# Performance work log

Hardware: AMD Instinct MI355X
Metric: run time of the kernel (lower is better)

The kernel has to match this reference:

```python
import jax, jax.numpy as jnp
import numpy as np

N, D_IN, D_OUT, H = 8192, 256, 128, 2
SLOPE = 0.2
EPS = 1e-5  # InstanceNorm2d default eps


def setup_inputs() -> dict:
    key = jax.random.key(0)
    ks = jax.random.split(key, 6)
    x = jax.random.normal(ks[0], (N, D_IN), dtype=jnp.float32)
    conn_mask = jnp.where(jax.random.uniform(ks[1], (N, N)) < 0.05, 0.0, -1e9).astype(jnp.float32)
    W = jax.random.normal(ks[2], (H, D_IN, D_OUT), dtype=jnp.float32) * 0.05
    a_src = jax.random.normal(ks[3], (H, D_OUT), dtype=jnp.float32) * 0.1
    a_tgt = jax.random.normal(ks[4], (H, D_OUT), dtype=jnp.float32) * 0.1
    W_res = jax.random.normal(ks[5], (D_OUT, D_IN), dtype=jnp.float32) * 0.05
    return {"x": x, "conn_mask": conn_mask, "W": W, "a_src": a_src, "a_tgt": a_tgt, "W_res": W_res}


def reference(x, conn_mask, W, a_src, a_tgt, W_res):
    # dropout is identity in eval mode
    proj = jnp.einsum('nd,hdf->hnf', x, W)                      # [H,N,F]
    s_src = jnp.einsum('hnf,hf->hn', proj, a_src)[:, :, None]   # [H,N,1]
    s_tgt = jnp.einsum('hnf,hf->hn', proj, a_tgt)[:, None, :]   # [H,1,N]
    scores = jax.nn.leaky_relu(s_src + s_tgt, negative_slope=SLOPE)  # [H,N,N]
    attn = jax.nn.softmax(conn_mask[None] + scores, axis=1)     # softmax over dim=1 as in torch code
    vals = jnp.einsum('hmn,hnf->hmf', attn, proj)               # bmm -> [H,N,F]
    vals = vals.mean(axis=0)                                    # head mean -> [N,F]
    # InstanceNorm2d(1, affine=False) over the whole [N,F] plane, biased variance
    mu = vals.mean()
    var = jnp.mean(jnp.square(vals - mu))
    vals_norm = (vals - mu) / jnp.sqrt(var + EPS)
    out = vals_norm + x @ W_res.T                               # residual projection (no bias)
    out = jax.nn.elu(out)
    return (out, conn_mask)
```

## Files before the change

kernel.cpp:

```cpp
#include <hip/hip_runtime.h>
#include <stdint.h>

#define NN   8192
#define DIN  256
#define FF   128
#define NF   (NN*FF)
#define SLOPE 0.2f
#define EPSI  1e-5f

typedef float vf4 __attribute__((ext_vector_type(4)));

#define OFF_PROJ   0
#define OFF_RESID  (2*NF)
#define OFF_PACKED (3*NF)
#define OFF_SS     (4*NF)
#define OFF_ST     (OFF_SS + 2*NN)
#define OFF_CSUM   (OFF_ST + 2*NN)
#define OFF_STATS  (OFF_CSUM + 2*NN)
#define OFF_NTAB   (OFF_STATS + 16)
#define OFF_VALS   (OFF_NTAB + 4*NN)
#define OFF_WT     (OFF_VALS + NF)

__device__ __forceinline__ float lrelu(float x) { return x >= 0.f ? x : SLOPE * x; }

__device__ __forceinline__ uint32_t bfpack(float a, float b) {
  uint32_t ua = __float_as_uint(a); ua += 0x7fffu + ((ua >> 16) & 1u);
  uint32_t ub = __float_as_uint(b); ub += 0x7fffu + ((ub >> 16) & 1u);
  return (ua >> 16) | (ub & 0xffff0000u);
}

__global__ __launch_bounds__(256) void k_wt(const float* __restrict__ wres, float* __restrict__ wt) {
  int i = blockIdx.x * 256 + threadIdx.x;
  int d = i >> 7, f = i & 127;
  wt[i] = wres[f * DIN + d];
}

__global__ __launch_bounds__(256) void k_gemm(const float* __restrict__ x, const float* __restrict__ Wh,
                                              const float* __restrict__ wt, float* __restrict__ proj,
                                              float* __restrict__ resid) {
  const int h = blockIdx.y;
  const float* __restrict__ Wsrc = (h < 2) ? (Wh + h * (DIN * FF)) : wt;
  float* __restrict__ outp = (h < 2) ? (proj + h * NF) : resid;
  const int row0 = blockIdx.x * 64;
  __shared__ float xs[64 * 68];
  const int tid = threadIdx.x;
  const int ft = tid & 15, rt = tid >> 4;
  const int f0 = ft * 8, r0 = rt * 4;
  float acc[4][8];
#pragma unroll
  for (int j = 0; j < 4; ++j)
#pragma unroll
    for (int k = 0; k < 8; ++k) acc[j][k] = 0.f;

  for (int kc = 0; kc < 4; ++kc) {
    const int d0 = kc * 64;
#pragma unroll
    for (int k2 = 0; k2 < 4; ++k2) {
      int i = tid * 4 + k2 * 1024;
      int r = i >> 6, dd = i & 63;
      *(float4*)&xs[r * 68 + dd] = *(const float4*)&x[(row0 + r) * DIN + d0 + dd];
    }
    __syncthreads();
#pragma unroll
    for (int g = 0; g < 16; ++g) {
      const int dd = g * 4;
      float xr[4][4];
#pragma unroll
      for (int j = 0; j < 4; ++j) {
        float4 t = *(const float4*)&xs[(r0 + j) * 68 + dd];
        xr[j][0] = t.x; xr[j][1] = t.y; xr[j][2] = t.z; xr[j][3] = t.w;
      }
#pragma unroll
      for (int i = 0; i < 4; ++i) {
        float4 wa = *(const float4*)&Wsrc[(d0 + dd + i) * FF + f0];
        float4 wb = *(const float4*)&Wsrc[(d0 + dd + i) * FF + f0 + 4];
#pragma unroll
        for (int j = 0; j < 4; ++j) {
          float xx = xr[j][i];
          acc[j][0] += xx * wa.x; acc[j][1] += xx * wa.y; acc[j][2] += xx * wa.z; acc[j][3] += xx * wa.w;
          acc[j][4] += xx * wb.x; acc[j][5] += xx * wb.y; acc[j][6] += xx * wb.z; acc[j][7] += xx * wb.w;
        }
      }
    }
    __syncthreads();
  }
#pragma unroll
  for (int j = 0; j < 4; ++j) {
    int row = row0 + r0 + j;
    *(float4*)&outp[row * FF + f0]     = make_float4(acc[j][0], acc[j][1], acc[j][2], acc[j][3]);
    *(float4*)&outp[row * FF + f0 + 4] = make_float4(acc[j][4], acc[j][5], acc[j][6], acc[j][7]);
  }
}

__global__ __launch_bounds__(256) void k_sprep(const float* __restrict__ proj, const float* __restrict__ a_src,
                                               const float* __restrict__ a_tgt, float* __restrict__ ss,
                                               float* __restrict__ st, uint32_t* __restrict__ packed) {
  int lane = threadIdx.x & 63, wid = threadIdx.x >> 6;
  int n = blockIdx.x * 4 + wid;
  float2 q0 = *(const float2*)&proj[n * FF + 2 * lane];
  float2 q1 = *(const float2*)&proj[NF + n * FF + 2 * lane];
  float2 as0 = *(const float2*)&a_src[2 * lane];
  float2 at0 = *(const float2*)&a_tgt[2 * lane];
  float2 as1 = *(const float2*)&a_src[FF + 2 * lane];
  float2 at1 = *(const float2*)&a_tgt[FF + 2 * lane];
  float v0 = q0.x * as0.x + q0.y * as0.y;
  float v1 = q0.x * at0.x + q0.y * at0.y;
  float v2 = q1.x * as1.x + q1.y * as1.y;
  float v3 = q1.x * at1.x + q1.y * at1.y;
#pragma unroll
  for (int o = 1; o < 64; o <<= 1) {
    v0 += __shfl_xor(v0, o); v1 += __shfl_xor(v1, o);
    v2 += __shfl_xor(v2, o); v3 += __shfl_xor(v3, o);
  }
  uint2 pk;
  pk.x = bfpack(q0.x, q1.x);
  pk.y = bfpack(q0.y, q1.y);
  *(uint2*)&packed[n * FF + 2 * lane] = pk;
  if (lane == 0) { ss[n] = v0; ss[NN + n] = v2; st[n] = v1; st[NN + n] = v3; }
}

__global__ __launch_bounds__(256) void k_scan(const float* __restrict__ mask, float* __restrict__ maskout,
                                              const float* __restrict__ ss, const float* __restrict__ st,
                                              float* __restrict__ csum, uint32_t* __restrict__ bitmask) {
  const int tid = threadIdx.x;
  const int lane = tid & 63, wv = tid >> 6;
  const int n = blockIdx.x * 256 + tid;
  const int m0 = blockIdx.y * 128;
  const int wbase = blockIdx.x * 8 + wv * 2;
  const float st0 = st[n], st1 = st[NN + n];
  float c0 = 0.f, c1 = 0.f;

  for (int i = 0; i < 128; i += 4) {
    float v[4];
#pragma unroll
    for (int r = 0; r < 4; ++r)
      v[r] = __builtin_nontemporal_load(&mask[(size_t)(m0 + i + r) * NN + n]);
#pragma unroll
    for (int r = 0; r < 4; ++r) {
      const int m = m0 + i + r;
      __builtin_nontemporal_store(v[r], &maskout[(size_t)m * NN + n]);
      bool e = v[r] > -0.5e9f;
      unsigned long long bm = __ballot(e);
      if (lane == 0)
        *(uint2*)&bitmask[m * 256 + wbase] = make_uint2((uint32_t)bm, (uint32_t)(bm >> 32));
      float w0 = __expf(lrelu(ss[m] + st0));
      float w1 = __expf(lrelu(ss[NN + m] + st1));
      c0 += e ? w0 : 0.f;
      c1 += e ? w1 : 0.f;
    }
  }
  atomicAdd(&csum[n], c0);
  atomicAdd(&csum[NN + n], c1);
}

__global__ __launch_bounds__(256) void k_ntab(const float* __restrict__ st, const float* __restrict__ csum,
                                              float4* __restrict__ ntab) {
  int i = blockIdx.x * 256 + threadIdx.x;
  ntab[i] = make_float4(st[i], st[NN + i], 1.f / csum[i], 1.f / csum[NN + i]);
}

__global__ __launch_bounds__(256) void k_vals(const uint32_t* __restrict__ bitmask, const uint32_t* __restrict__ packed,
                                              const float4* __restrict__ ntab, const float* __restrict__ ss,
                                              float* __restrict__ vals, float* __restrict__ stats) {
  __shared__ uint16_t el[4][1024];
  const int lane = threadIdx.x & 63, wid = threadIdx.x >> 6;
  const int m = blockIdx.x * 4 + wid;

  uint4 wv = ((const uint4*)(bitmask + m * 256))[lane];
  uint32_t wd[4] = {wv.x, wv.y, wv.z, wv.w};
  int cnt = __popc(wd[0]) + __popc(wd[1]) + __popc(wd[2]) + __popc(wd[3]);
  int pre = cnt;
#pragma unroll
  for (int o = 1; o < 64; o <<= 1) { int t = __shfl_up(pre, o); if (lane >= o) pre += t; }
  int nE = __shfl(pre, 63);
  int base = pre - cnt;
#pragma unroll
  for (int u = 0; u < 4; ++u) {
    uint32_t w = wd[u];
    int nbase = lane * 128 + u * 32;
    while (w) {
      int b = __builtin_ctz(w); w &= w - 1;
      if (base < 1024) el[wid][base] = (uint16_t)(nbase + b);
      ++base;
    }
  }
  if (nE > 1024) nE = 1024;
  __builtin_amdgcn_wave_barrier();

  const float ss0 = ss[m], ss1 = ss[NN + m];
  float a00 = 0.f, a01 = 0.f, a10 = 0.f, a11 = 0.f;
  const char* __restrict__ pb = (const char*)packed;
  const int lane8 = 8 * lane;
  for (int t = 0; t < nE; t += 64) {
    int e = t + lane;
    float w0 = 0.f, w1 = 0.f; uint32_t off = 0;
    if (e < nE) {
      int n = el[wid][e];
      float4 tb = ntab[n];
      w0 = __expf(lrelu(ss0 + tb.x)) * tb.z;
      w1 = __expf(lrelu(ss1 + tb.y)) * tb.w;
      off = (uint32_t)n << 9;
    }
#pragma unroll 1
    for (int k2 = 0; k2 < 4; ++k2) {
      uint2 d[16];
#pragma unroll
      for (int j = 0; j < 16; ++j) {
        uint32_t so = __builtin_amdgcn_readlane(off, k2 * 16 + j);
        d[j] = *(const uint2*)(pb + so + lane8);
      }
#pragma unroll
      for (int j = 0; j < 16; ++j) {
        float sw0 = __uint_as_float(__builtin_amdgcn_readlane(__float_as_uint(w0), k2 * 16 + j));
        float sw1 = __uint_as_float(__builtin_amdgcn_readlane(__float_as_uint(w1), k2 * 16 + j));
        uint32_t pa = d[j].x, pc = d[j].y;
        a00 += sw0 * __uint_as_float(pa << 16);
        a10 += sw1 * __uint_as_float(pa & 0xffff0000u);
        a01 += sw0 * __uint_as_float(pc << 16);
        a11 += sw1 * __uint_as_float(pc & 0xffff0000u);
      }
    }
  }

  float v0 = 0.5f * (a00 + a10), v1 = 0.5f * (a01 + a11);
  *(float2*)&vals[m * FF + 2 * lane] = make_float2(v0, v1);
  float s = v0 + v1, q = v0 * v0 + v1 * v1;
#pragma unroll
  for (int o = 1; o < 64; o <<= 1) { s += __shfl_xor(s, o); q += __shfl_xor(q, o); }
  if (lane == 0) { atomicAdd(stats, s); atomicAdd(stats + 1, q); }
}

__global__ __launch_bounds__(256) void k_final(const float* __restrict__ vals, const float* __restrict__ resid,
                                               const float* __restrict__ stats, float* __restrict__ out) {
  int i = (blockIdx.x * 256 + threadIdx.x) * 4;
  float mu = stats[0] * (1.f / NF);
  float var = stats[1] * (1.f / NF) - mu * mu;
  float rs = rsqrtf(var + EPSI);
  float4 v = *(const float4*)&vals[i];
  float4 r = *(const float4*)&resid[i];
  float t0 = (v.x - mu) * rs + r.x;
  float t1 = (v.y - mu) * rs + r.y;
  float t2 = (v.z - mu) * rs + r.z;
  float t3 = (v.w - mu) * rs + r.w;
  float4 o;
  o.x = t0 > 0.f ? t0 : expm1f(t0);
  o.y = t1 > 0.f ? t1 : expm1f(t1);
  o.z = t2 > 0.f ? t2 : expm1f(t2);
  o.w = t3 > 0.f ? t3 : expm1f(t3);
  *(float4*)&out[i] = o;
}

extern "C" void kernel_launch(void* const* d_in, const int* in_sizes, int n_in,
                              void* d_out, int out_size, void* d_ws, size_t ws_size,
                              hipStream_t stream) {
  const float* x     = (const float*)d_in[0];
  const float* mask  = (const float*)d_in[1];
  const float* W     = (const float*)d_in[2];
  const float* a_src = (const float*)d_in[3];
  const float* a_tgt = (const float*)d_in[4];
  const float* wres  = (const float*)d_in[5];
  float* out = (float*)d_out;
  float* wsf = (float*)d_ws;

  float*    proj    = wsf + OFF_PROJ;
  uint32_t* bitmask = (uint32_t*)(wsf + OFF_PROJ);
  float*    resid   = wsf + OFF_RESID;
  uint32_t* packed  = (uint32_t*)(wsf + OFF_PACKED);
  float*    ss      = wsf + OFF_SS;
  float*    st      = wsf + OFF_ST;
  float*    csum    = wsf + OFF_CSUM;
  float*    stats   = wsf + OFF_STATS;
  float4*   ntab    = (float4*)(wsf + OFF_NTAB);
  float*    vals    = wsf + OFF_VALS;
  float*    wt      = wsf + OFF_WT;

  (void)hipMemsetAsync(csum, 0, (2 * NN + 16) * sizeof(float), stream);

  hipLaunchKernelGGL(k_wt,    dim3(DIN * FF / 256), dim3(256), 0, stream, wres, wt);
  hipLaunchKernelGGL(k_gemm,  dim3(NN / 64, 3),     dim3(256), 0, stream, x, W, wt, proj, resid);
  hipLaunchKernelGGL(k_sprep, dim3(NN / 4),         dim3(256), 0, stream, proj, a_src, a_tgt, ss, st, packed);
  hipLaunchKernelGGL(k_scan,  dim3(NN / 256, NN / 128), dim3(256), 0, stream, mask, out + NF, ss, st, csum, bitmask);
  hipLaunchKernelGGL(k_ntab,  dim3(NN / 256),       dim3(256), 0, stream, st, csum, ntab);
  hipLaunchKernelGGL(k_vals,  dim3(NN / 4),         dim3(256), 0, stream, bitmask, packed, ntab, ss, vals, stats);
  hipLaunchKernelGGL(k_final, dim3(NF / 1024),      dim3(256), 0, stream, vals, resid, stats, out);
}
```

Measured before the change: 769.2 us.

## Double-buffer gathered rows into LDS via async global_load_lds in k_vals

In k_vals, the gather of packed bf16 projection rows now goes through direct global-to-LDS loads into a per-wave double buffer, with explicit waitcnt fences so the next sub-block's loads overlap the FMAs on the current one. Per-edge weights are staged in LDS rather than broadcast with readlane. In k_scan, the ss values are loaded once per lane and broadcast with readlane instead of being reloaded every row, and the unroll grows from 4 to 8. This adds LDS pressure, which may cut occupancy, and relies on hand-tuned waitcnt encodings that are easy to get wrong.

```diff
diff --git a/kernel.cpp b/kernel.cpp
--- a/kernel.cpp
+++ b/kernel.cpp
@@ -9,6 +9,15 @@
 #define EPSI  1e-5f
 
 typedef float vf4 __attribute__((ext_vector_type(4)));
+
+#if __has_builtin(__builtin_amdgcn_sched_barrier)
+#define SCHED_FENCE() __builtin_amdgcn_sched_barrier(0)
+#else
+#define SCHED_FENCE() asm volatile("" ::: "memory")
+#endif
+
+#define WAITCNT_VM16_LGKM0 0x4070
+#define WAITCNT_VM0_LGKM0  0x0070
 
 #define OFF_PROJ   0
 #define OFF_RESID  (2*NF)
@@ -128,23 +137,30 @@
   const int m0 = blockIdx.y * 128;
   const int wbase = blockIdx.x * 8 + wv * 2;
   const float st0 = st[n], st1 = st[NN + n];
+  const float ssA = ss[m0 + lane],      ssB = ss[m0 + 64 + lane];
+  const float ssC = ss[NN + m0 + lane], ssD = ss[NN + m0 + 64 + lane];
   float c0 = 0.f, c1 = 0.f;
 
-  for (int i = 0; i < 128; i += 4) {
-    float v[4];
-#pragma unroll
-    for (int r = 0; r < 4; ++r)
+  for (int i = 0; i < 128; i += 8) {
+    float v[8];
+#pragma unroll
+    for (int r = 0; r < 8; ++r)
       v[r] = __builtin_nontemporal_load(&mask[(size_t)(m0 + i + r) * NN + n]);
 #pragma unroll
-    for (int r = 0; r < 4; ++r) {
+    for (int r = 0; r < 8; ++r) {
       const int m = m0 + i + r;
       __builtin_nontemporal_store(v[r], &maskout[(size_t)m * NN + n]);
       bool e = v[r] > -0.5e9f;
       unsigned long long bm = __ballot(e);
       if (lane == 0)
         *(uint2*)&bitmask[m * 256 + wbase] = make_uint2((uint32_t)bm, (uint32_t)(bm >> 32));
-      float w0 = __expf(lrelu(ss[m] + st0));
-      float w1 = __expf(lrelu(ss[NN + m] + st1));
+      const int ri = i + r;
+      float s0 = __uint_as_float(__builtin_amdgcn_readlane(
+                   __float_as_uint(ri < 64 ? ssA : ssB), ri & 63));
+      float s1 = __uint_as_float(__builtin_amdgcn_readlane(
+                   __float_as_uint(ri < 64 ? ssC : ssD), ri & 63));
+      float w0 = __expf(lrelu(s0 + st0));
+      float w1 = __expf(lrelu(s1 + st1));
       c0 += e ? w0 : 0.f;
       c1 += e ? w1 : 0.f;
     }
@@ -163,6 +179,8 @@
                                               const float4* __restrict__ ntab, const float* __restrict__ ss,
                                               float* __restrict__ vals, float* __restrict__ stats) {
   __shared__ uint16_t el[4][1024];
+  __shared__ uint32_t dbuf[4][2][8 * 128];
+  __shared__ float2   wbuf[4][64];
   const int lane = threadIdx.x & 63, wid = threadIdx.x >> 6;
   const int m = blockIdx.x * 4 + wid;
 
@@ -190,7 +208,9 @@
   const float ss0 = ss[m], ss1 = ss[NN + m];
   float a00 = 0.f, a01 = 0.f, a10 = 0.f, a11 = 0.f;
   const char* __restrict__ pb = (const char*)packed;
-  const int lane8 = 8 * lane;
+  uint32_t* __restrict__ db0 = &dbuf[wid][0][0];
+  uint32_t* __restrict__ db1 = &dbuf[wid][1][0];
+
   for (int t = 0; t < nE; t += 64) {
     int e = t + lane;
     float w0 = 0.f, w1 = 0.f; uint32_t off = 0;
@@ -201,25 +221,55 @@
       w1 = __expf(lrelu(ss1 + tb.y)) * tb.w;
       off = (uint32_t)n << 9;
     }
+    wbuf[wid][lane] = make_float2(w0, w1);
+    __builtin_amdgcn_wave_barrier();
+
+#define ISSUE_SB(sb)                                                                   \
+    {                                                                                  \
+      uint32_t* dst = ((sb) & 1) ? db1 : db0;                                          \
+      _Pragma("unroll")                                                                \
+      for (int j = 0; j < 8; ++j) {                                                    \
+        uint32_t so = __builtin_amdgcn_readlane(off, (sb) * 8 + j);                    \
+        const uint32_t* g = (const uint32_t*)(pb + so) + lane;                         \
+        __builtin_amdgcn_global_load_lds(                                              \
+            (const __attribute__((address_space(1))) uint32_t*)g,                      \
+            (__attribute__((address_space(3))) uint32_t*)&dst[j * 128], 4, 0, 0);      \
+        __builtin_amdgcn_global_load_lds(                                              \
+            (const __attribute__((address_space(1))) uint32_t*)(g + 64),               \
+            (__attribute__((address_space(3))) uint32_t*)&dst[j * 128 + 64], 4, 0, 0); \
+      }                                                                                \
+    }
+
+    ISSUE_SB(0)
 #pragma unroll 1
-    for (int k2 = 0; k2 < 4; ++k2) {
-      uint2 d[16];
-#pragma unroll
-      for (int j = 0; j < 16; ++j) {
-        uint32_t so = __builtin_amdgcn_readlane(off, k2 * 16 + j);
-        d[j] = *(const uint2*)(pb + so + lane8);
+    for (int sb = 0; sb < 8; ++sb) {
+      if (sb < 7) {
+        switch (sb + 1) {
+          case 1: ISSUE_SB(1) break; case 2: ISSUE_SB(2) break; case 3: ISSUE_SB(3) break;
+          case 4: ISSUE_SB(4) break; case 5: ISSUE_SB(5) break; case 6: ISSUE_SB(6) break;
+          case 7: ISSUE_SB(7) break;
+        }
+        SCHED_FENCE();
+        __builtin_amdgcn_s_waitcnt(WAITCNT_VM16_LGKM0);
+        SCHED_FENCE();
+      } else {
+        SCHED_FENCE();
+        __builtin_amdgcn_s_waitcnt(WAITCNT_VM0_LGKM0);
+        SCHED_FENCE();
       }
-#pragma unroll
-      for (int j = 0; j < 16; ++j) {
-        float sw0 = __uint_as_float(__builtin_amdgcn_readlane(__float_as_uint(w0), k2 * 16 + j));
-        float sw1 = __uint_as_float(__builtin_amdgcn_readlane(__float_as_uint(w1), k2 * 16 + j));
-        uint32_t pa = d[j].x, pc = d[j].y;
-        a00 += sw0 * __uint_as_float(pa << 16);
-        a10 += sw1 * __uint_as_float(pa & 0xffff0000u);
-        a01 += sw0 * __uint_as_float(pc << 16);
-        a11 += sw1 * __uint_as_float(pc & 0xffff0000u);
+      const uint32_t* src = (sb & 1) ? db1 : db0;
+#pragma unroll
+      for (int j = 0; j < 8; ++j) {
+        float2 w = wbuf[wid][sb * 8 + j];
+        uint2 d = *(const uint2*)&src[j * 128 + 2 * lane];
+        a00 += w.x * __uint_as_float(d.x << 16);
+        a10 += w.y * __uint_as_float(d.x & 0xffff0000u);
+        a01 += w.x * __uint_as_float(d.y << 16);
+        a11 += w.y * __uint_as_float(d.y & 0xffff0000u);
       }
     }
+    __builtin_amdgcn_wave_barrier();
+#undef ISSUE_SB
   }
 
   float v0 = 0.5f * (a00 + a10), v1 = 0.5f * (a01 + a11);
```

Result: slower. 858.2 us (+11.6%).

## Vectorize mask scan to float4 per thread with interleaved bitmask layout

Applied to the files above, without the earlier changes.

The scan kernel now loads and stores the 256MB connectivity mask as float4 per thread instead of scalar floats, with each block covering 1024 columns by 64 rows. It reads the per-row source scores through readlane broadcasts. Because each ballot now covers every fourth column, the bitmask layout changes, and the vals kernel's index decoding is updated to match. A scheduling barrier is also added between the gather loads and the FMAs in k_vals. The aim is to raise memory-transaction efficiency on the dominant mask copy and scan, at the cost of a more complex bitmask encoding and more atomics per thread.

```diff
diff --git a/kernel.cpp b/kernel.cpp
--- a/kernel.cpp
+++ b/kernel.cpp
@@ -9,6 +9,12 @@
 #define EPSI  1e-5f
 
 typedef float vf4 __attribute__((ext_vector_type(4)));
+
+#if __has_builtin(__builtin_amdgcn_sched_barrier)
+#define SCHED_FENCE() __builtin_amdgcn_sched_barrier(0)
+#else
+#define SCHED_FENCE() asm volatile("" ::: "memory")
+#endif
 
 #define OFF_PROJ   0
 #define OFF_RESID  (2*NF)
@@ -124,33 +130,47 @@
                                               float* __restrict__ csum, uint32_t* __restrict__ bitmask) {
   const int tid = threadIdx.x;
   const int lane = tid & 63, wv = tid >> 6;
-  const int n = blockIdx.x * 256 + tid;
-  const int m0 = blockIdx.y * 128;
-  const int wbase = blockIdx.x * 8 + wv * 2;
-  const float st0 = st[n], st1 = st[NN + n];
-  float c0 = 0.f, c1 = 0.f;
-
-  for (int i = 0; i < 128; i += 4) {
-    float v[4];
-#pragma unroll
-    for (int r = 0; r < 4; ++r)
-      v[r] = __builtin_nontemporal_load(&mask[(size_t)(m0 + i + r) * NN + n]);
-#pragma unroll
-    for (int r = 0; r < 4; ++r) {
+  const int nb = blockIdx.x * 1024 + tid * 4;
+  const int C = blockIdx.x * 4 + wv;
+  const int m0 = blockIdx.y * 64;
+  const vf4 st0 = *(const vf4*)&st[nb];
+  const vf4 st1 = *(const vf4*)&st[NN + nb];
+  const float ssA = ss[m0 + lane];
+  const float ssC = ss[NN + m0 + lane];
+  float c0[4] = {0.f, 0.f, 0.f, 0.f}, c1[4] = {0.f, 0.f, 0.f, 0.f};
+
+  for (int i = 0; i < 64; i += 8) {
+    vf4 v[8];
+#pragma unroll
+    for (int r = 0; r < 8; ++r)
+      v[r] = *(const vf4*)&mask[(size_t)(m0 + i + r) * NN + nb];
+#pragma unroll
+    for (int r = 0; r < 8; ++r) {
       const int m = m0 + i + r;
-      __builtin_nontemporal_store(v[r], &maskout[(size_t)m * NN + n]);
-      bool e = v[r] > -0.5e9f;
-      unsigned long long bm = __ballot(e);
-      if (lane == 0)
-        *(uint2*)&bitmask[m * 256 + wbase] = make_uint2((uint32_t)bm, (uint32_t)(bm >> 32));
-      float w0 = __expf(lrelu(ss[m] + st0));
-      float w1 = __expf(lrelu(ss[NN + m] + st1));
-      c0 += e ? w0 : 0.f;
-      c1 += e ? w1 : 0.f;
-    }
-  }
-  atomicAdd(&csum[n], c0);
-  atomicAdd(&csum[NN + n], c1);
+      __builtin_nontemporal_store(v[r], (vf4*)&maskout[(size_t)m * NN + nb]);
+      unsigned long long bms[4];
+      bool e[4];
+#pragma unroll
+      for (int j = 0; j < 4; ++j) { e[j] = v[r][j] > -0.5e9f; bms[j] = __ballot(e[j]); }
+      if (lane < 8)
+        bitmask[m * 256 + C * 8 + lane] = (uint32_t)(bms[lane >> 1] >> ((lane & 1) * 32));
+      const int ri = i + r;
+      float s0 = __uint_as_float(__builtin_amdgcn_readlane(__float_as_uint(ssA), ri));
+      float s1 = __uint_as_float(__builtin_amdgcn_readlane(__float_as_uint(ssC), ri));
+#pragma unroll
+      for (int j = 0; j < 4; ++j) {
+        float w0 = __expf(lrelu(s0 + st0[j]));
+        float w1 = __expf(lrelu(s1 + st1[j]));
+        c0[j] += e[j] ? w0 : 0.f;
+        c1[j] += e[j] ? w1 : 0.f;
+      }
+    }
+  }
+#pragma unroll
+  for (int j = 0; j < 4; ++j) {
+    atomicAdd(&csum[nb + j], c0[j]);
+    atomicAdd(&csum[NN + nb + j], c1[j]);
+  }
 }
 
 __global__ __launch_bounds__(256) void k_ntab(const float* __restrict__ st, const float* __restrict__ csum,
@@ -177,10 +197,11 @@
 #pragma unroll
   for (int u = 0; u < 4; ++u) {
     uint32_t w = wd[u];
-    int nbase = lane * 128 + u * 32;
+    int widx = 4 * lane + u;
+    int nbase = (widx >> 3) * 256 + (widx & 1) * 128 + ((widx >> 1) & 3);
     while (w) {
       int b = __builtin_ctz(w); w &= w - 1;
-      if (base < 1024) el[wid][base] = (uint16_t)(nbase + b);
+      if (base < 1024) el[wid][base] = (uint16_t)(nbase + 4 * b);
       ++base;
     }
   }
@@ -204,15 +225,17 @@
 #pragma unroll 1
     for (int k2 = 0; k2 < 4; ++k2) {
       uint2 d[16];
+      const int kb = k2 * 16;
 #pragma unroll
       for (int j = 0; j < 16; ++j) {
-        uint32_t so = __builtin_amdgcn_readlane(off, k2 * 16 + j);
+        uint32_t so = __builtin_amdgcn_readlane(off, kb + j);
         d[j] = *(const uint2*)(pb + so + lane8);
       }
+      SCHED_FENCE();
 #pragma unroll
       for (int j = 0; j < 16; ++j) {
-        float sw0 = __uint_as_float(__builtin_amdgcn_readlane(__float_as_uint(w0), k2 * 16 + j));
-        float sw1 = __uint_as_float(__builtin_amdgcn_readlane(__float_as_uint(w1), k2 * 16 + j));
+        float sw0 = __uint_as_float(__builtin_amdgcn_readlane(__float_as_uint(w0), kb + j));
+        float sw1 = __uint_as_float(__builtin_amdgcn_readlane(__float_as_uint(w1), kb + j));
         uint32_t pa = d[j].x, pc = d[j].y;
         a00 += sw0 * __uint_as_float(pa << 16);
         a10 += sw1 * __uint_as_float(pa & 0xffff0000u);
@@ -279,7 +302,7 @@
   hipLaunchKernelGGL(k_wt,    dim3(DIN * FF / 256), dim3(256), 0, stream, wres, wt);
   hipLaunchKernelGGL(k_gemm,  dim3(NN / 64, 3),     dim3(256), 0, stream, x, W, wt, proj, resid);
   hipLaunchKernelGGL(k_sprep, dim3(NN / 4),         dim3(256), 0, stream, proj, a_src, a_tgt, ss, st, packed);
-  hipLaunchKernelGGL(k_scan,  dim3(NN / 256, NN / 128), dim3(256), 0, stream, mask, out + NF, ss, st, csum, bitmask);
+  hipLaunchKernelGGL(k_scan,  dim3(NN / 1024, NN / 64), dim3(256), 0, stream, mask, out + NF, ss, st, csum, bitmask);
   hipLaunchKernelGGL(k_ntab,  dim3(NN / 256),       dim3(256), 0, stream, st, csum, ntab);
   hipLaunchKernelGGL(k_vals,  dim3(NN / 4),         dim3(256), 0, stream, bitmask, packed, ntab, ss, vals, stats);
   hipLaunchKernelGGL(k_final, dim3(NF / 1024),      dim3(256), 0, stream, vals, resid, stats, out);
```

Result: slower. 852.4 us (+10.8%).

## Replace sparse gather aggregation with dense bf16 MFMA over transposed projections

Applied to the files above, without the earlier changes.

The attention aggregation kernel drops the per-row edge-list gather and instead computes a dense masked product with bf16 MFMA instructions. Each block covers 32 rows, builds masked exp weights into LDS and streams a new transposed, head-split copy of the projections, which a new transpose kernel produces. The scan kernel also reads source scores through readlane from registers instead of per-row global loads, and unrolls 8 rows per iteration. The dense form does about 20 times the useful work at 5% density and rounds the attention weights to bf16. With only 256 blocks of 128 threads it may leave much of the GPU idle.

```diff
diff --git a/kernel.cpp b/kernel.cpp
--- a/kernel.cpp
+++ b/kernel.cpp
@@ -9,6 +9,8 @@
 #define EPSI  1e-5f
 
 typedef float vf4 __attribute__((ext_vector_type(4)));
+typedef short bf16x8 __attribute__((ext_vector_type(8)));
+typedef float f32x4 __attribute__((ext_vector_type(4)));
 
 #define OFF_PROJ   0
 #define OFF_RESID  (2*NF)
@@ -20,6 +22,7 @@
 #define OFF_NTAB   (OFF_STATS + 16)
 #define OFF_VALS   (OFF_NTAB + 4*NN)
 #define OFF_WT     (OFF_VALS + NF)
+#define OFF_PT2    (OFF_WT + DIN*FF)
 
 __device__ __forceinline__ float lrelu(float x) { return x >= 0.f ? x : SLOPE * x; }
 
@@ -119,6 +122,30 @@
   if (lane == 0) { ss[n] = v0; ss[NN + n] = v2; st[n] = v1; st[NN + n] = v3; }
 }
 
+__global__ __launch_bounds__(256) void k_tpose(const uint32_t* __restrict__ packed, uint32_t* __restrict__ pt2) {
+  __shared__ uint32_t sb[32][129];
+  const int t = threadIdx.x, c = blockIdx.x;
+  const int nl = t >> 3, fb = (t & 7) * 16;
+#pragma unroll
+  for (int i = 0; i < 4; ++i) {
+    uint4 v = *(const uint4*)&packed[(c * 32 + nl) * FF + fb + i * 4];
+    sb[nl][fb + i * 4] = v.x; sb[nl][fb + i * 4 + 1] = v.y;
+    sb[nl][fb + i * 4 + 2] = v.z; sb[nl][fb + i * 4 + 3] = v.w;
+  }
+  __syncthreads();
+  const int h = t >> 7, f = t & 127;
+  uint32_t wbuf[16];
+#pragma unroll
+  for (int p = 0; p < 16; ++p) {
+    uint32_t a = sb[2 * p][f], b = sb[2 * p + 1][f];
+    wbuf[p] = h ? ((a >> 16) | (b & 0xffff0000u)) : ((a & 0xffffu) | (b << 16));
+  }
+  uint32_t* dst = pt2 + ((c * 2 + h) * 128 + f) * 16;
+#pragma unroll
+  for (int i = 0; i < 4; ++i)
+    *(uint4*)&dst[i * 4] = make_uint4(wbuf[i * 4], wbuf[i * 4 + 1], wbuf[i * 4 + 2], wbuf[i * 4 + 3]);
+}
+
 __global__ __launch_bounds__(256) void k_scan(const float* __restrict__ mask, float* __restrict__ maskout,
                                               const float* __restrict__ ss, const float* __restrict__ st,
                                               float* __restrict__ csum, uint32_t* __restrict__ bitmask) {
@@ -128,23 +155,30 @@
   const int m0 = blockIdx.y * 128;
   const int wbase = blockIdx.x * 8 + wv * 2;
   const float st0 = st[n], st1 = st[NN + n];
+  const float ssA = ss[m0 + lane],      ssB = ss[m0 + 64 + lane];
+  const float ssC = ss[NN + m0 + lane], ssD = ss[NN + m0 + 64 + lane];
   float c0 = 0.f, c1 = 0.f;
 
-  for (int i = 0; i < 128; i += 4) {
-    float v[4];
-#pragma unroll
-    for (int r = 0; r < 4; ++r)
+  for (int i = 0; i < 128; i += 8) {
+    float v[8];
+#pragma unroll
+    for (int r = 0; r < 8; ++r)
       v[r] = __builtin_nontemporal_load(&mask[(size_t)(m0 + i + r) * NN + n]);
 #pragma unroll
-    for (int r = 0; r < 4; ++r) {
+    for (int r = 0; r < 8; ++r) {
       const int m = m0 + i + r;
       __builtin_nontemporal_store(v[r], &maskout[(size_t)m * NN + n]);
       bool e = v[r] > -0.5e9f;
       unsigned long long bm = __ballot(e);
       if (lane == 0)
         *(uint2*)&bitmask[m * 256 + wbase] = make_uint2((uint32_t)bm, (uint32_t)(bm >> 32));
-      float w0 = __expf(lrelu(ss[m] + st0));
-      float w1 = __expf(lrelu(ss[NN + m] + st1));
+      const int ri = i + r;
+      float s0 = __uint_as_float(__builtin_amdgcn_readlane(
+                   __float_as_uint(ri < 64 ? ssA : ssB), ri & 63));
+      float s1 = __uint_as_float(__builtin_amdgcn_readlane(
+                   __float_as_uint(ri < 64 ? ssC : ssD), ri & 63));
+      float w0 = __expf(lrelu(s0 + st0));
+      float w1 = __expf(lrelu(s1 + st1));
       c0 += e ? w0 : 0.f;
       c1 += e ? w1 : 0.f;
     }
@@ -159,75 +193,82 @@
   ntab[i] = make_float4(st[i], st[NN + i], 1.f / csum[i], 1.f / csum[NN + i]);
 }
 
-__global__ __launch_bounds__(256) void k_vals(const uint32_t* __restrict__ bitmask, const uint32_t* __restrict__ packed,
+__global__ __launch_bounds__(128) void k_vals(const uint32_t* __restrict__ bitmask, const uint32_t* __restrict__ pt2,
                                               const float4* __restrict__ ntab, const float* __restrict__ ss,
                                               float* __restrict__ vals, float* __restrict__ stats) {
-  __shared__ uint16_t el[4][1024];
-  const int lane = threadIdx.x & 63, wid = threadIdx.x >> 6;
-  const int m = blockIdx.x * 4 + wid;
-
-  uint4 wv = ((const uint4*)(bitmask + m * 256))[lane];
-  uint32_t wd[4] = {wv.x, wv.y, wv.z, wv.w};
-  int cnt = __popc(wd[0]) + __popc(wd[1]) + __popc(wd[2]) + __popc(wd[3]);
-  int pre = cnt;
-#pragma unroll
-  for (int o = 1; o < 64; o <<= 1) { int t = __shfl_up(pre, o); if (lane >= o) pre += t; }
-  int nE = __shfl(pre, 63);
-  int base = pre - cnt;
-#pragma unroll
-  for (int u = 0; u < 4; ++u) {
-    uint32_t w = wd[u];
-    int nbase = lane * 128 + u * 32;
-    while (w) {
-      int b = __builtin_ctz(w); w &= w - 1;
-      if (base < 1024) el[wid][base] = (uint16_t)(nbase + b);
-      ++base;
-    }
-  }
-  if (nE > 1024) nE = 1024;
-  __builtin_amdgcn_wave_barrier();
-
-  const float ss0 = ss[m], ss1 = ss[NN + m];
-  float a00 = 0.f, a01 = 0.f, a10 = 0.f, a11 = 0.f;
-  const char* __restrict__ pb = (const char*)packed;
-  const int lane8 = 8 * lane;
-  for (int t = 0; t < nE; t += 64) {
-    int e = t + lane;
-    float w0 = 0.f, w1 = 0.f; uint32_t off = 0;
-    if (e < nE) {
-      int n = el[wid][e];
-      float4 tb = ntab[n];
-      w0 = __expf(lrelu(ss0 + tb.x)) * tb.z;
-      w1 = __expf(lrelu(ss1 + tb.y)) * tb.w;
-      off = (uint32_t)n << 9;
-    }
-#pragma unroll 1
-    for (int k2 = 0; k2 < 4; ++k2) {
-      uint2 d[16];
-#pragma unroll
-      for (int j = 0; j < 16; ++j) {
-        uint32_t so = __builtin_amdgcn_readlane(off, k2 * 16 + j);
-        d[j] = *(const uint2*)(pb + so + lane8);
-      }
-#pragma unroll
-      for (int j = 0; j < 16; ++j) {
-        float sw0 = __uint_as_float(__builtin_amdgcn_readlane(__float_as_uint(w0), k2 * 16 + j));
-        float sw1 = __uint_as_float(__builtin_amdgcn_readlane(__float_as_uint(w1), k2 * 16 + j));
-        uint32_t pa = d[j].x, pc = d[j].y;
-        a00 += sw0 * __uint_as_float(pa << 16);
-        a10 += sw1 * __uint_as_float(pa & 0xffff0000u);
-        a01 += sw0 * __uint_as_float(pc << 16);
-        a11 += sw1 * __uint_as_float(pc & 0xffff0000u);
-      }
-    }
-  }
-
-  float v0 = 0.5f * (a00 + a10), v1 = 0.5f * (a01 + a11);
-  *(float2*)&vals[m * FF + 2 * lane] = make_float2(v0, v1);
-  float s = v0 + v1, q = v0 * v0 + v1 * v1;
-#pragma unroll
-  for (int o = 1; o < 64; o <<= 1) { s += __shfl_xor(s, o); q += __shfl_xor(q, o); }
-  if (lane == 0) { atomicAdd(stats, s); atomicAdd(stats + 1, q); }
+  __shared__ short lds_B[2][128][40];
+  __shared__ short lds_A[2][32][40];
+  const int t = threadIdx.x;
+  const int lane = t & 63, wid = t >> 6;
+  const int m0 = blockIdx.x * 32;
+  const int q = lane >> 4, col = lane & 15;
+  const int n2 = t & 15, mg = t >> 4;
+
+  float ssm0[4], ssm1[4];
+#pragma unroll
+  for (int p = 0; p < 4; ++p) {
+    ssm0[p] = ss[m0 + mg + 8 * p];
+    ssm1[p] = ss[NN + m0 + mg + 8 * p];
+  }
+
+  f32x4 acc[8];
+#pragma unroll
+  for (int i = 0; i < 8; ++i) acc[i] = (f32x4){0.f, 0.f, 0.f, 0.f};
+
+  uint32_t* ldsb_w = (uint32_t*)&lds_B[0][0][0];
+
+  for (int step = 0; step < NN / 32; ++step) {
+    const int n0 = step * 32;
+    const uint32_t* src = pt2 + step * 4096;
+#pragma unroll
+    for (int i = 0; i < 8; ++i) {
+      uint4 v = *(const uint4*)&src[t * 4 + i * 512];
+      int row = (t >> 2) + i * 32, c4 = (t & 3) * 4;
+      *(uint4*)&ldsb_w[row * 20 + c4] = v;
+    }
+    float4 na = ntab[n0 + 2 * n2];
+    float4 nb = ntab[n0 + 2 * n2 + 1];
+#pragma unroll
+    for (int p = 0; p < 4; ++p) {
+      const int ml = mg + 8 * p;
+      uint32_t bw = bitmask[(size_t)(m0 + ml) * 256 + (n0 >> 5)];
+      float e0a = __expf(lrelu(ssm0[p] + na.x)) * na.z;
+      float e1a = __expf(lrelu(ssm1[p] + na.y)) * na.w;
+      float e0b = __expf(lrelu(ssm0[p] + nb.x)) * nb.z;
+      float e1b = __expf(lrelu(ssm1[p] + nb.y)) * nb.w;
+      bool b0 = (bw >> (2 * n2)) & 1, b1 = (bw >> (2 * n2 + 1)) & 1;
+      e0a = b0 ? e0a : 0.f; e1a = b0 ? e1a : 0.f;
+      e0b = b1 ? e0b : 0.f; e1b = b1 ? e1b : 0.f;
+      *(uint32_t*)&lds_A[0][ml][2 * n2] = bfpack(e0a, e0b);
+      *(uint32_t*)&lds_A[1][ml][2 * n2] = bfpack(e1a, e1b);
+    }
+    __syncthreads();
+    bf16x8 a0 = *(const bf16x8*)&lds_A[0][wid * 16 + col][q * 8];
+    bf16x8 a1 = *(const bf16x8*)&lds_A[1][wid * 16 + col][q * 8];
+#pragma unroll
+    for (int ft = 0; ft < 8; ++ft) {
+      bf16x8 b0 = *(const bf16x8*)&lds_B[0][ft * 16 + col][q * 8];
+      acc[ft] = __builtin_amdgcn_mfma_f32_16x16x32_bf16(a0, b0, acc[ft], 0, 0, 0);
+      bf16x8 b1 = *(const bf16x8*)&lds_B[1][ft * 16 + col][q * 8];
+      acc[ft] = __builtin_amdgcn_mfma_f32_16x16x32_bf16(a1, b1, acc[ft], 0, 0, 0);
+    }
+    __syncthreads();
+  }
+
+  float s = 0.f, qq = 0.f;
+#pragma unroll
+  for (int ft = 0; ft < 8; ++ft) {
+#pragma unroll
+    for (int r = 0; r < 4; ++r) {
+      int mrow = m0 + wid * 16 + q * 4 + r;
+      float v = 0.5f * acc[ft][r];
+      vals[mrow * FF + ft * 16 + col] = v;
+      s += v; qq += v * v;
+    }
+  }
+#pragma unroll
+  for (int o = 1; o < 64; o <<= 1) { s += __shfl_xor(s, o); qq += __shfl_xor(qq, o); }
+  if (lane == 0) { atomicAdd(stats, s); atomicAdd(stats + 1, qq); }
 }
 
 __global__ __launch_bounds__(256) void k_final(const float* __restrict__ vals, const float* __restrict__ resid,
@@ -273,14 +314,16 @@
   float4*   ntab    = (float4*)(wsf + OFF_NTAB);
   float*    vals    = wsf + OFF_VALS;
   float*    wt      = wsf + OFF_WT;
+  uint32_t* pt2     = (uint32_t*)(wsf + OFF_PT2);
 
   (void)hipMemsetAsync(csum, 0, (2 * NN + 16) * sizeof(float), stream);
 
   hipLaunchKernelGGL(k_wt,    dim3(DIN * FF / 256), dim3(256), 0, stream, wres, wt);
   hipLaunchKernelGGL(k_gemm,  dim3(NN / 64, 3),     dim3(256), 0, stream, x, W, wt, proj, resid);
   hipLaunchKernelGGL(k_sprep, dim3(NN / 4),         dim3(256), 0, stream, proj, a_src, a_tgt, ss, st, packed);
+  hipLaunchKernelGGL(k_tpose, dim3(NN / 32),        dim3(256), 0, stream, packed, pt2);
   hipLaunchKernelGGL(k_scan,  dim3(NN / 256, NN / 128), dim3(256), 0, stream, mask, out + NF, ss, st, csum, bitmask);
   hipLaunchKernelGGL(k_ntab,  dim3(NN / 256),       dim3(256), 0, stream, st, csum, ntab);
-  hipLaunchKernelGGL(k_vals,  dim3(NN / 4),         dim3(256), 0, stream, bitmask, packed, ntab, ss, vals, stats);
+  hipLaunchKernelGGL(k_vals,  dim3(NN / 32),        dim3(128), 0, stream, bitmask, pt2, ntab, ss, vals, stats);
   hipLaunchKernelGGL(k_final, dim3(NF / 1024),      dim3(256), 0, stream, vals, resid, stats, out);
 }
```

Result: slower. 840.0 us (+9.2%).
